# Performance work log

Hardware: AMD Instinct MI355X
Metric: run time of the kernel (lower is better)

Reference implementation:

```python
import jax, jax.numpy as jnp
import numpy as np
from jax import lax

B, T_SRC, I, H, L, O = 1024, 1024, 64, 512, 64, 1


def _lstm_cell(x, h, c, W_ih, W_hh, b):
    # PyTorch gate order: i, f, g, o. b = b_ih + b_hh (same math).
    gates = x @ W_ih.T + h @ W_hh.T + b  # (B, 4H)
    i, f, g, o = jnp.split(gates, 4, axis=-1)
    c_new = jax.nn.sigmoid(f) * c + jax.nn.sigmoid(i) * jnp.tanh(g)
    h_new = jax.nn.sigmoid(o) * jnp.tanh(c_new)
    return h_new, c_new


def setup_inputs() -> dict:
    key = jax.random.key(0)
    ks = jax.random.split(key, 16)
    s_e = 1.0 / np.sqrt(H)
    inp = {
        "src": jax.random.normal(ks[0], (B, T_SRC, I), dtype=jnp.float32),
        "eps": jax.random.normal(ks[1], (B, L), dtype=jnp.float32),
        "tgt_len": 1024,
        # encoder LSTM
        "W_ih_e": jax.random.uniform(ks[2], (4 * H, I), jnp.float32, -s_e, s_e),
        "W_hh_e": jax.random.uniform(ks[3], (4 * H, H), jnp.float32, -s_e, s_e),
        "b_e": jax.random.uniform(ks[4], (4 * H,), jnp.float32, -s_e, s_e),
        # fc_mu / fc_logvar
        "W_mu": jax.random.uniform(ks[5], (L, H), jnp.float32, -s_e, s_e),
        "b_mu": jax.random.uniform(ks[6], (L,), jnp.float32, -s_e, s_e),
        "W_lv": jax.random.uniform(ks[7], (L, H), jnp.float32, -s_e, s_e),
        "b_lv": jax.random.uniform(ks[8], (L,), jnp.float32, -s_e, s_e),
        # z -> h0, c0
        "W_zh": jax.random.uniform(ks[9], (H, L), jnp.float32, -s_e, s_e),
        "b_zh": jax.random.uniform(ks[10], (H,), jnp.float32, -s_e, s_e),
        "W_zc": jax.random.uniform(ks[11], (H, L), jnp.float32, -s_e, s_e),
        "b_zc": jax.random.uniform(ks[12], (H,), jnp.float32, -s_e, s_e),
        # decoder LSTM + fc_out
        "W_ih_d": jax.random.uniform(ks[13], (4 * H, O), jnp.float32, -s_e, s_e),
        "W_hh_d": jax.random.uniform(ks[14], (4 * H, H), jnp.float32, -s_e, s_e),
        "b_d": jax.random.uniform(ks[15], (4 * H,), jnp.float32, -s_e, s_e),
        "W_out": jax.random.uniform(jax.random.fold_in(key, 100), (O, H), jnp.float32, -s_e, s_e),
        "b_out": jax.random.uniform(jax.random.fold_in(key, 101), (O,), jnp.float32, -s_e, s_e),
    }
    return inp


def reference(src, eps, W_ih_e, W_hh_e, b_e, W_mu, b_mu, W_lv, b_lv,
              W_zh, b_zh, W_zc, b_zc, W_ih_d, W_hh_d, b_d, W_out, b_out,
              tgt_len):
    batch = src.shape[0]
    hid = W_hh_e.shape[1]

    # ---- Encoder: LSTM over src, take final hidden state ----
    def enc_step(carry, x_t):
        h, c = carry
        h, c = _lstm_cell(x_t, h, c, W_ih_e, W_hh_e, b_e)
        return (h, c), None

    h0 = jnp.zeros((batch, hid), src.dtype)
    (h_n, _), _ = lax.scan(enc_step, (h0, h0), jnp.swapaxes(src, 0, 1))

    mu = h_n @ W_mu.T + b_mu          # (B, L)
    logvar = h_n @ W_lv.T + b_lv      # (B, L)

    # ---- Reparameterize ----
    z = mu + eps * jnp.exp(0.5 * logvar)

    h_d = jnp.tanh(z @ W_zh.T + b_zh)
    c_d = jnp.tanh(z @ W_zc.T + b_zc)
    x0 = jnp.zeros((batch, W_ih_d.shape[1]), src.dtype)  # (B, output_size)

    def dec_step(carry, _):
        h, c, x = carry
        h, c = _lstm_cell(x, h, c, W_ih_d, W_hh_d, b_d)
        out = h @ W_out.T + b_out     # (B, O)
        return (h, c, out), out

    _, outs = lax.scan(dec_step, (h_d, c_d, x0), None, length=tgt_len)
    recon = jnp.swapaxes(outs, 0, 1)  # (B, tgt_len, O)
    return recon, mu, logvar
```

## Files before the change

### kernel.cpp

```cpp
#include <hip/hip_runtime.h>


#define NWG  256
#define NTHR 256

typedef __attribute__((ext_vector_type(8))) short short8;
typedef __attribute__((ext_vector_type(4))) float f32x4;
typedef __attribute__((ext_vector_type(4))) unsigned int u32x4;

constexpr int Bt = 1024;
constexpr int Tt = 1024;
constexpr int In = 64;
constexpr int Hn = 512;
constexpr int Ln = 64;
constexpr int KE = In + Hn;
constexpr int BSE = KE + 8;
constexpr int KD = Hn;
constexpr int BSD = KD + 8;
constexpr int LDS_BYTES = 128 * BSE * 2;
constexpr int AP_MI = 16 * Hn;

__device__ __forceinline__ float bf2f(unsigned short s){
  unsigned u = ((unsigned)s) << 16; float f; __builtin_memcpy(&f, &u, 4); return f;
}
__device__ __forceinline__ unsigned short f2bf(float f){
  unsigned u; __builtin_memcpy(&u, &f, 4);
  u += 0x7FFFu + ((u >> 16) & 1u);
  return (unsigned short)(u >> 16);
}
__device__ __forceinline__ float sigm(float x){ return 1.0f / (1.0f + __expf(-x)); }
__device__ __forceinline__ float tanh_(float x){ float e = __expf(2.0f * x); return 1.0f - 2.0f / (e + 1.0f); }

__device__ __forceinline__ u32x4 ldcc(const void* p){
  u32x4 r;
  asm volatile("global_load_dwordx4 %0, %1, off sc0 sc1" : "=&v"(r) : "v"(p) : "memory");
  return r;
}
__device__ __forceinline__ float ld32cc(const void* p){
  float r;
  asm volatile("global_load_dword %0, %1, off sc0 sc1" : "=&v"(r) : "v"(p) : "memory");
  return r;
}
__device__ __forceinline__ void st16cc(void* p, unsigned v){
  asm volatile("global_store_short %0, %1, off sc0 sc1" :: "v"(p), "v"(v) : "memory");
}
__device__ __forceinline__ void st32cc(void* p, float v){
  asm volatile("global_store_dword %0, %1, off sc0 sc1" :: "v"(p), "v"(v) : "memory");
}
__device__ __forceinline__ void st128cc(void* p, u32x4 v){
  asm volatile("global_store_dwordx4 %0, %1, off sc0 sc1" :: "v"(p), "v"(v) : "memory");
}

__device__ __forceinline__ void group_sync(unsigned* cnt, unsigned target){
  asm volatile("s_waitcnt vmcnt(0)" ::: "memory");
  __syncthreads();
  if (threadIdx.x == 0){
    __hip_atomic_fetch_add(cnt, 1u, __ATOMIC_RELAXED, __HIP_MEMORY_SCOPE_AGENT);
    while (__hip_atomic_load(cnt, __ATOMIC_RELAXED, __HIP_MEMORY_SCOPE_AGENT) < target)
      __builtin_amdgcn_s_sleep(2);
  }
  __syncthreads();
}

#define SB0 __builtin_amdgcn_sched_barrier(0)

#define LOADC(P, CBASE) do{                                              \
    _Pragma("unroll") for (int ti_ = 0; ti_ < 4; ++ti_){                 \
      A[P][ti_][0] = ldcc(ap + (CBASE) + ti_ * 32);                      \
      A[P][ti_][1] = ldcc(ap + AP_MI + (CBASE) + ti_ * 32);              \
    } }while(0)

#define WAITC(P, N) do{                                                  \
    asm volatile("s_waitcnt vmcnt(" N ")"                                \
      : "+v"(A[P][0][0]), "+v"(A[P][0][1]), "+v"(A[P][1][0]),            \
        "+v"(A[P][1][1]), "+v"(A[P][2][0]), "+v"(A[P][2][1]),            \
        "+v"(A[P][3][0]), "+v"(A[P][3][1]) :: "memory");                 \
    SB0; }while(0)

#define COMPC(P, K0, BB, BS) do{                                         \
    _Pragma("unroll") for (int ti_ = 0; ti_ < 4; ++ti_){                 \
      short8 a0_ = __builtin_bit_cast(short8, A[P][ti_][0]);             \
      short8 a1_ = __builtin_bit_cast(short8, A[P][ti_][1]);             \
      _Pragma("unroll") for (int ni_ = 0; ni_ < 4; ++ni_){               \
        short8 bv_ = *(const short8*)((BB) + ni_ * 16 * (BS) + (K0) + ti_ * 32); \
        acc[0][ni_] = __builtin_amdgcn_mfma_f32_16x16x32_bf16(a0_, bv_, acc[0][ni_], 0, 0, 0); \
        acc[1][ni_] = __builtin_amdgcn_mfma_f32_16x16x32_bf16(a1_, bv_, acc[1][ni_], 0, 0, 0); \
      } } }while(0)

extern "C" __global__ void __launch_bounds__(NTHR, 1)
vae_fused(const float* __restrict__ src, const float* __restrict__ eps,
          const float* __restrict__ Wih_e, const float* __restrict__ Whh_e, const float* __restrict__ b_e,
          const float* __restrict__ Wmu, const float* __restrict__ bmu,
          const float* __restrict__ Wlv, const float* __restrict__ blv,
          const float* __restrict__ Wzh, const float* __restrict__ bzh,
          const float* __restrict__ Wzc, const float* __restrict__ bzc,
          const float* __restrict__ Wih_d, const float* __restrict__ Whh_d, const float* __restrict__ b_d,
          const float* __restrict__ Wout, const float* __restrict__ bout,
          float* __restrict__ out,
          unsigned* cnt_all, unsigned short* hbuf0, unsigned short* hbuf1,
          float* zbuf, float* obuf)
{
  const int tid  = threadIdx.x;
  const int wg   = blockIdx.x;
  const int lane = tid & 63;
  const int wave = tid >> 6;
  const int wm   = wave >> 1, wn = wave & 1;
  const int mt   = wg & 15;
  const int nt   = wg >> 4;
  unsigned* cnt  = cnt_all + mt * 32;
  unsigned bars  = 0;

  extern __shared__ short bpanel[];

  const int l15   = lane & 15;
  const int l4    = lane >> 4;
  const int kq    = l4 * 8;
  const int jcol  = nt * 32 + wn * 16 + l15;
  const int arow0 = mt * 64 + wm * 32 + l15;
  const int brow0 = mt * 64 + wm * 32 + l4 * 4;

  {
    const int idx = nt * NTHR + tid;
    const u32x4 z = {0u, 0u, 0u, 0u};
    st128cc(hbuf0 + (size_t)(mt * 64 + (idx >> 6)) * Hn + (idx & 63) * 8, z);
  }
  for (int idx = tid; idx < 128 * KE; idx += NTHR){
    int q = idx / KE;
    int k = idx - q * KE;
    int gate = (q >> 4) & 3, jl = q & 15, wnn = (q >> 6) & 1;
    int j = nt * 32 + wnn * 16 + jl;
    int r = gate * Hn + j;
    float v = (k < In) ? Wih_e[r * In + k] : Whh_e[(size_t)r * Hn + (k - In)];
    bpanel[q * BSE + k] = (short)f2bf(v);
  }
  float biasr[4], wihr[4];
  #pragma unroll
  for (int ni = 0; ni < 4; ++ni) biasr[ni] = b_e[ni * Hn + jcol];
  bars += 16; group_sync(cnt, bars);

  float c[2][4] = {{0.f,0.f,0.f,0.f},{0.f,0.f,0.f,0.f}};
  const f32x4 fz = {0.f, 0.f, 0.f, 0.f};
  u32x4 A[2][4][2];

  for (int t = 0; t < Tt; ++t){
    const unsigned short* hs = (t & 1) ? hbuf1 : hbuf0;
    unsigned short*       hd = (t & 1) ? hbuf0 : hbuf1;
    f32x4 acc[2][4];
    #pragma unroll
    for (int mi = 0; mi < 2; ++mi)
      #pragma unroll
      for (int ni = 0; ni < 4; ++ni) acc[mi][ni] = fz;

    const short* bbase = bpanel + (wn * 64 + l15) * BSE + kq;

    short8 sa[2][2];
    #pragma unroll
    for (int mi = 0; mi < 2; ++mi){
      const float* sp = src + ((size_t)(arow0 + mi * 16) * Tt + t) * In + kq;
      f32x4 f0 = *(const f32x4*)sp;
      f32x4 f1 = *(const f32x4*)(sp + 4);
      f32x4 f2 = *(const f32x4*)(sp + 32);
      f32x4 f3 = *(const f32x4*)(sp + 36);
      short8 a0, a1;
      #pragma unroll
      for (int e = 0; e < 4; ++e){
        a0[e] = (short)f2bf(f0[e]); a0[4 + e] = (short)f2bf(f1[e]);
        a1[e] = (short)f2bf(f2[e]); a1[4 + e] = (short)f2bf(f3[e]);
      }
      sa[mi][0] = a0; sa[mi][1] = a1;
    }

    const unsigned short* ap = hs + (size_t)arow0 * Hn + kq;
    LOADC(0, 0); LOADC(1, 128);

    #pragma unroll
    for (int kk = 0; kk < 2; ++kk)
      #pragma unroll
      for (int ni = 0; ni < 4; ++ni){
        short8 bv = *(const short8*)(bbase + ni * 16 * BSE + kk * 32);
        acc[0][ni] = __builtin_amdgcn_mfma_f32_16x16x32_bf16(sa[0][kk], bv, acc[0][ni], 0, 0, 0);
        acc[1][ni] = __builtin_amdgcn_mfma_f32_16x16x32_bf16(sa[1][kk], bv, acc[1][ni], 0, 0, 0);
      }

    WAITC(0, "8"); COMPC(0, In + 0,   bbase, BSE);
    LOADC(0, 256);
    WAITC(1, "8"); COMPC(1, In + 128, bbase, BSE);
    LOADC(1, 384);
    WAITC(0, "8"); COMPC(0, In + 256, bbase, BSE);
    WAITC(1, "0"); COMPC(1, In + 384, bbase, BSE);

    #pragma unroll
    for (int mi = 0; mi < 2; ++mi){
      #pragma unroll
      for (int r = 0; r < 4; ++r){
        float gi = acc[mi][0][r] + biasr[0];
        float gf = acc[mi][1][r] + biasr[1];
        float gg = acc[mi][2][r] + biasr[2];
        float go = acc[mi][3][r] + biasr[3];
        float cn = sigm(gf) * c[mi][r] + sigm(gi) * tanh_(gg);
        c[mi][r] = cn;
        float hn = sigm(go) * tanh_(cn);
        st16cc(hd + (size_t)(brow0 + mi * 16 + r) * Hn + jcol, (unsigned)f2bf(hn));
      }
    }
    bars += 16; group_sync(cnt, bars);
  }

  {
    const int lt = nt * NTHR + tid;
    const int b  = mt * 64 + (lt >> 6);
    const int l  = lt & 63;
    const unsigned short* hp = hbuf0 + (size_t)b * Hn;
    const float* wmrow = Wmu + l * Hn;
    const float* wlrow = Wlv + l * Hn;
    float smu = 0.f, slv = 0.f;
    for (int jj = 0; jj < Hn; jj += 32){
      u32x4 v0 = ldcc(hp + jj), v1 = ldcc(hp + jj + 8), v2 = ldcc(hp + jj + 16), v3 = ldcc(hp + jj + 24);
      asm volatile("s_waitcnt vmcnt(0)" : "+v"(v0), "+v"(v1), "+v"(v2), "+v"(v3) :: "memory");
      short8 h0 = __builtin_bit_cast(short8, v0);
      short8 h1 = __builtin_bit_cast(short8, v1);
      short8 h2 = __builtin_bit_cast(short8, v2);
      short8 h3 = __builtin_bit_cast(short8, v3);
      #pragma unroll
      for (int e = 0; e < 8; ++e){
        float f0 = bf2f((unsigned short)h0[e]), f1 = bf2f((unsigned short)h1[e]);
        float f2 = bf2f((unsigned short)h2[e]), f3 = bf2f((unsigned short)h3[e]);
        smu = __builtin_fmaf(f0, wmrow[jj + e], smu);      slv = __builtin_fmaf(f0, wlrow[jj + e], slv);
        smu = __builtin_fmaf(f1, wmrow[jj + 8 + e], smu);  slv = __builtin_fmaf(f1, wlrow[jj + 8 + e], slv);
        smu = __builtin_fmaf(f2, wmrow[jj + 16 + e], smu); slv = __builtin_fmaf(f2, wlrow[jj + 16 + e], slv);
        smu = __builtin_fmaf(f3, wmrow[jj + 24 + e], smu); slv = __builtin_fmaf(f3, wlrow[jj + 24 + e], slv);
      }
    }
    smu += bmu[l]; slv += blv[l];
    out[(size_t)Bt * Tt + (size_t)b * Ln + l] = smu;
    out[(size_t)Bt * Tt + (size_t)Bt * Ln + (size_t)b * Ln + l] = slv;
    st32cc(zbuf + (size_t)b * Ln + l, smu + eps[(size_t)b * Ln + l] * __expf(0.5f * slv));
  }
  bars += 16; group_sync(cnt, bars);

  for (int idx = tid; idx < 128 * KD; idx += NTHR){
    int q = idx >> 9, k = idx & 511;
    int gate = (q >> 4) & 3, jl = q & 15, wnn = (q >> 6) & 1;
    int j = nt * 32 + wnn * 16 + jl;
    bpanel[q * BSD + k] = (short)f2bf(Whh_d[(size_t)(gate * Hn + j) * Hn + k]);
  }
  #pragma unroll
  for (int ni = 0; ni < 4; ++ni){
    biasr[ni] = b_d[ni * Hn + jcol];
    wihr[ni]  = Wih_d[ni * Hn + jcol];
  }
  const float woutr = Wout[jcol];
  const float bov   = bout[0];
  #pragma unroll
  for (int mi = 0; mi < 2; ++mi){
    #pragma unroll
    for (int r = 0; r < 4; ++r){
      int b = brow0 + mi * 16 + r;
      const float* zp  = zbuf + (size_t)b * Ln;
      const float* whr = Wzh + jcol * Ln;
      const float* wcr = Wzc + jcol * Ln;
      float sh = bzh[jcol], sc = bzc[jcol];
      for (int e0 = 0; e0 < Ln; e0 += 16){
        u32x4 z0 = ldcc(zp + e0), z1 = ldcc(zp + e0 + 4), z2 = ldcc(zp + e0 + 8), z3 = ldcc(zp + e0 + 12);
        asm volatile("s_waitcnt vmcnt(0)" : "+v"(z0), "+v"(z1), "+v"(z2), "+v"(z3) :: "memory");
        f32x4 zf0 = __builtin_bit_cast(f32x4, z0);
        f32x4 zf1 = __builtin_bit_cast(f32x4, z1);
        f32x4 zf2 = __builtin_bit_cast(f32x4, z2);
        f32x4 zf3 = __builtin_bit_cast(f32x4, z3);
        #pragma unroll
        for (int e = 0; e < 4; ++e){
          sh = __builtin_fmaf(zf0[e], whr[e0 + e], sh);      sc = __builtin_fmaf(zf0[e], wcr[e0 + e], sc);
          sh = __builtin_fmaf(zf1[e], whr[e0 + 4 + e], sh);  sc = __builtin_fmaf(zf1[e], wcr[e0 + 4 + e], sc);
          sh = __builtin_fmaf(zf2[e], whr[e0 + 8 + e], sh);  sc = __builtin_fmaf(zf2[e], wcr[e0 + 8 + e], sc);
          sh = __builtin_fmaf(zf3[e], whr[e0 + 12 + e], sh); sc = __builtin_fmaf(zf3[e], wcr[e0 + 12 + e], sc);
        }
      }
      c[mi][r] = tanh_(sc);
      st16cc(hbuf0 + (size_t)b * Hn + jcol, (unsigned)f2bf(tanh_(sh)));
    }
  }
  if (nt == 0 && tid < 3 * 64)
    st32cc(obuf + (tid >> 6) * Bt + mt * 64 + (tid & 63), bov);
  bars += 16; group_sync(cnt, bars);

  for (int t = 0; t < Tt; ++t){
    const unsigned short* hs = (t & 1) ? hbuf1 : hbuf0;
    unsigned short*       hd = (t & 1) ? hbuf0 : hbuf1;
    float*       oacc  = obuf + (t % 3) * Bt;
    const float* oread = obuf + ((t + 2) % 3) * Bt;
    float*       orst  = obuf + ((t + 1) % 3) * Bt;

    if (nt == 0){
      if (t > 0 && tid < 64){
        float v = ld32cc(oread + mt * 64 + tid);
        asm volatile("s_waitcnt vmcnt(0)" : "+v"(v) :: "memory");
        out[(size_t)(mt * 64 + tid) * Tt + (t - 1)] = v;
      }
      if (tid < 64) st32cc(orst + mt * 64 + tid, bov);
    }

    float xv[2][4];
    #pragma unroll
    for (int mi = 0; mi < 2; ++mi)
      #pragma unroll
      for (int r = 0; r < 4; ++r)
        xv[mi][r] = ld32cc(oread + brow0 + mi * 16 + r);

    f32x4 acc[2][4];
    #pragma unroll
    for (int mi = 0; mi < 2; ++mi)
      #pragma unroll
      for (int ni = 0; ni < 4; ++ni) acc[mi][ni] = fz;

    const short* bbase = bpanel + (wn * 64 + l15) * BSD + kq;
    const unsigned short* ap = hs + (size_t)arow0 * Hn + kq;

    LOADC(0, 0); LOADC(1, 128);
    WAITC(0, "8"); COMPC(0, 0,   bbase, BSD);
    LOADC(0, 256);
    WAITC(1, "8"); COMPC(1, 128, bbase, BSD);
    LOADC(1, 384);
    WAITC(0, "8"); COMPC(0, 256, bbase, BSD);
    WAITC(1, "0"); COMPC(1, 384, bbase, BSD);

    asm volatile("s_waitcnt vmcnt(0)"
      : "+v"(xv[0][0]), "+v"(xv[0][1]), "+v"(xv[0][2]), "+v"(xv[0][3]),
        "+v"(xv[1][0]), "+v"(xv[1][1]), "+v"(xv[1][2]), "+v"(xv[1][3]) :: "memory");

    #pragma unroll
    for (int mi = 0; mi < 2; ++mi){
      #pragma unroll
      for (int r = 0; r < 4; ++r){
        float x = (t == 0) ? 0.f : xv[mi][r];
        float gi = acc[mi][0][r] + biasr[0] + x * wihr[0];
        float gf = acc[mi][1][r] + biasr[1] + x * wihr[1];
        float gg = acc[mi][2][r] + biasr[2] + x * wihr[2];
        float go = acc[mi][3][r] + biasr[3] + x * wihr[3];
        float cn = sigm(gf) * c[mi][r] + sigm(gi) * tanh_(gg);
        c[mi][r] = cn;
        float hn = sigm(go) * tanh_(cn);
        int b = brow0 + mi * 16 + r;
        st16cc(hd + (size_t)b * Hn + jcol, (unsigned)f2bf(hn));
        float pv = hn * woutr;
        pv += __shfl_xor(pv, 1);
        pv += __shfl_xor(pv, 2);
        pv += __shfl_xor(pv, 4);
        pv += __shfl_xor(pv, 8);
        if (l15 == 0)
          __hip_atomic_fetch_add(&oacc[b], pv, __ATOMIC_RELAXED, __HIP_MEMORY_SCOPE_AGENT);
      }
    }
    bars += 16; group_sync(cnt, bars);
  }
  if (nt == 0 && tid < 64){
    float v = ld32cc(obuf + 0 * Bt + mt * 64 + tid);
    asm volatile("s_waitcnt vmcnt(0)" : "+v"(v) :: "memory");
    out[(size_t)(mt * 64 + tid) * Tt + (Tt - 1)] = v;
  }
}

extern "C" void kernel_launch(void* const* d_in, const int* in_sizes, int n_in,
                              void* d_out, int out_size, void* d_ws, size_t ws_size,
                              hipStream_t stream){
  (void)in_sizes; (void)n_in; (void)out_size; (void)ws_size;
  const float* src   = (const float*)d_in[0];
  const float* eps   = (const float*)d_in[1];
  const float* Wih_e = (const float*)d_in[3];
  const float* Whh_e = (const float*)d_in[4];
  const float* b_e   = (const float*)d_in[5];
  const float* Wmu   = (const float*)d_in[6];
  const float* bmu   = (const float*)d_in[7];
  const float* Wlv   = (const float*)d_in[8];
  const float* blv   = (const float*)d_in[9];
  const float* Wzh   = (const float*)d_in[10];
  const float* bzh   = (const float*)d_in[11];
  const float* Wzc   = (const float*)d_in[12];
  const float* bzc   = (const float*)d_in[13];
  const float* Wih_d = (const float*)d_in[14];
  const float* Whh_d = (const float*)d_in[15];
  const float* b_d   = (const float*)d_in[16];
  const float* Wout  = (const float*)d_in[17];
  const float* bout  = (const float*)d_in[18];

  char* ws = (char*)d_ws;
  unsigned*       cnt  = (unsigned*)ws;
  unsigned short* h0   = (unsigned short*)(ws + 4096);
  unsigned short* h1   = (unsigned short*)(ws + 4096 + 1048576);
  float*          zbuf = (float*)(ws + 4096 + 2 * 1048576);
  float*          obuf = (float*)(ws + 4096 + 2 * 1048576 + 262144);

  hipFuncSetAttribute((const void*)vae_fused,
                      hipFuncAttributeMaxDynamicSharedMemorySize, LDS_BYTES);
  hipMemsetAsync(cnt, 0, 2048, stream);
  hipLaunchKernelGGL(vae_fused, dim3(NWG), dim3(NTHR), LDS_BYTES, stream,
                     src, eps, Wih_e, Whh_e, b_e, Wmu, bmu, Wlv, blv,
                     Wzh, bzh, Wzc, bzc, Wih_d, Whh_d, b_d, Wout, bout,
                     (float*)d_out, cnt, h0, h1, zbuf, obuf);
}
```

Baseline: 16.65 ms.

## Detect same-XCD groups to relax cache coherence bits; issue all h loads upfront

At startup each workgroup records its XCC id and checks whether all 16 workgroups sharing an M-tile sit on the same XCD. If they do, the hidden-state loads and stores drop the sc1 system-coherence bit and keep only sc0, so they can be served from the shared L2 instead of bypassing it. The kernel body is templated on this flag. The h-state loads are also issued as four chunks up front, rather than in two double-buffered pairs, and use immediate offsets; src loads become inline asm so they overlap with the h loads. This uses more registers, and if workgroups from one group land on different XCDs the kernel falls back to the fully coherent path.

```diff
diff --git a/kernel.cpp b/kernel.cpp
--- a/kernel.cpp
+++ b/kernel.cpp
@@ -8,11 +8,7 @@
 typedef __attribute__((ext_vector_type(4))) float f32x4;
 typedef __attribute__((ext_vector_type(4))) unsigned int u32x4;
 
-constexpr int Bt = 1024;
-constexpr int Tt = 1024;
-constexpr int In = 64;
-constexpr int Hn = 512;
-constexpr int Ln = 64;
+constexpr int Bt = 1024, Tt = 1024, In = 64, Hn = 512, Ln = 64;
 constexpr int KE = In + Hn;
 constexpr int BSE = KE + 8;
 constexpr int KD = Hn;
@@ -20,6 +16,8 @@
 constexpr int LDS_BYTES = 128 * BSE * 2;
 constexpr int AP_MI = 16 * Hn;
 
+template<bool B> struct BoolC { static constexpr bool value = B; };
+
 __device__ __forceinline__ float bf2f(unsigned short s){
   unsigned u = ((unsigned)s) << 16; float f; __builtin_memcpy(&f, &u, 4); return f;
 }
@@ -31,24 +29,58 @@
 __device__ __forceinline__ float sigm(float x){ return 1.0f / (1.0f + __expf(-x)); }
 __device__ __forceinline__ float tanh_(float x){ float e = __expf(2.0f * x); return 1.0f - 2.0f / (e + 1.0f); }
 
-__device__ __forceinline__ u32x4 ldcc(const void* p){
+template<bool SAME, int OFF>
+__device__ __forceinline__ u32x4 ldA(const void* p){
   u32x4 r;
-  asm volatile("global_load_dwordx4 %0, %1, off sc0 sc1" : "=&v"(r) : "v"(p) : "memory");
+  if constexpr (SAME) asm volatile("global_load_dwordx4 %0, %1, off offset:%c2 sc0" : "=&v"(r) : "v"(p), "i"(OFF));
+  else                asm volatile("global_load_dwordx4 %0, %1, off offset:%c2 sc0 sc1" : "=&v"(r) : "v"(p), "i"(OFF));
   return r;
 }
-__device__ __forceinline__ float ld32cc(const void* p){
+template<int OFF>
+__device__ __forceinline__ u32x4 ldP(const void* p){
+  u32x4 r;
+  asm volatile("global_load_dwordx4 %0, %1, off offset:%c2" : "=&v"(r) : "v"(p), "i"(OFF));
+  return r;
+}
+template<bool SAME>
+__device__ __forceinline__ float ld32w(const void* p){
   float r;
+  if constexpr (SAME) asm volatile("global_load_dword %0, %1, off sc0" : "=&v"(r) : "v"(p));
+  else                asm volatile("global_load_dword %0, %1, off sc0 sc1" : "=&v"(r) : "v"(p));
+  asm volatile("s_waitcnt vmcnt(0)" : "+v"(r));
+  return r;
+}
+template<bool SAME>
+__device__ __forceinline__ void st16(void* p, unsigned v){
+  if constexpr (SAME) asm volatile("global_store_short %0, %1, off sc0" :: "v"(p), "v"(v) : "memory");
+  else                asm volatile("global_store_short %0, %1, off sc0 sc1" :: "v"(p), "v"(v) : "memory");
+}
+template<bool SAME>
+__device__ __forceinline__ void st32(void* p, float v){
+  if constexpr (SAME) asm volatile("global_store_dword %0, %1, off sc0" :: "v"(p), "v"(v) : "memory");
+  else                asm volatile("global_store_dword %0, %1, off sc0 sc1" :: "v"(p), "v"(v) : "memory");
+}
+template<bool SAME>
+__device__ __forceinline__ void st128(void* p, u32x4 v){
+  if constexpr (SAME) asm volatile("global_store_dwordx4 %0, %1, off sc0" :: "v"(p), "v"(v) : "memory");
+  else                asm volatile("global_store_dwordx4 %0, %1, off sc0 sc1" :: "v"(p), "v"(v) : "memory");
+}
+__device__ __forceinline__ void stP32(void* p, float v){
+  asm volatile("global_store_dword %0, %1, off" :: "v"(p), "v"(v) : "memory");
+}
+template<bool SAME>
+__device__ __forceinline__ void atomAddF(float* p, float v){
+  if constexpr (SAME) asm volatile("global_atomic_add_f32 %0, %1, off" :: "v"(p), "v"(v) : "memory");
+  else                asm volatile("global_atomic_add_f32 %0, %1, off sc1" :: "v"(p), "v"(v) : "memory");
+}
+__device__ __forceinline__ unsigned ldMall(const unsigned* p){
+  unsigned r;
   asm volatile("global_load_dword %0, %1, off sc0 sc1" : "=&v"(r) : "v"(p) : "memory");
+  asm volatile("s_waitcnt vmcnt(0)" : "+v"(r) :: "memory");
   return r;
 }
-__device__ __forceinline__ void st16cc(void* p, unsigned v){
-  asm volatile("global_store_short %0, %1, off sc0 sc1" :: "v"(p), "v"(v) : "memory");
-}
-__device__ __forceinline__ void st32cc(void* p, float v){
+__device__ __forceinline__ void stMall(unsigned* p, unsigned v){
   asm volatile("global_store_dword %0, %1, off sc0 sc1" :: "v"(p), "v"(v) : "memory");
-}
-__device__ __forceinline__ void st128cc(void* p, u32x4 v){
-  asm volatile("global_store_dwordx4 %0, %1, off sc0 sc1" :: "v"(p), "v"(v) : "memory");
 }
 
 __device__ __forceinline__ void group_sync(unsigned* cnt, unsigned target){
@@ -62,27 +94,25 @@
   __syncthreads();
 }
 
-#define SB0 __builtin_amdgcn_sched_barrier(0)
-
-#define LOADC(P, CBASE) do{                                              \
-    _Pragma("unroll") for (int ti_ = 0; ti_ < 4; ++ti_){                 \
-      A[P][ti_][0] = ldcc(ap + (CBASE) + ti_ * 32);                      \
-      A[P][ti_][1] = ldcc(ap + AP_MI + (CBASE) + ti_ * 32);              \
-    } }while(0)
-
-#define WAITC(P, N) do{                                                  \
-    asm volatile("s_waitcnt vmcnt(" N ")"                                \
-      : "+v"(A[P][0][0]), "+v"(A[P][0][1]), "+v"(A[P][1][0]),            \
-        "+v"(A[P][1][1]), "+v"(A[P][2][0]), "+v"(A[P][2][1]),            \
-        "+v"(A[P][3][0]), "+v"(A[P][3][1]) :: "memory");                 \
-    SB0; }while(0)
-
-#define COMPC(P, K0, BB, BS) do{                                         \
-    _Pragma("unroll") for (int ti_ = 0; ti_ < 4; ++ti_){                 \
-      short8 a0_ = __builtin_bit_cast(short8, A[P][ti_][0]);             \
-      short8 a1_ = __builtin_bit_cast(short8, A[P][ti_][1]);             \
-      _Pragma("unroll") for (int ni_ = 0; ni_ < 4; ++ni_){               \
-        short8 bv_ = *(const short8*)((BB) + ni_ * 16 * (BS) + (K0) + ti_ * 32); \
+template<bool SAME, int CB>
+__device__ __forceinline__ void loadChunk(const unsigned short* a0, const unsigned short* a1,
+                                          u32x4 (&d)[4][2]){
+  d[0][0] = ldA<SAME, (CB +  0) * 2>(a0);  d[0][1] = ldA<SAME, (CB +  0) * 2>(a1);
+  d[1][0] = ldA<SAME, (CB + 32) * 2>(a0);  d[1][1] = ldA<SAME, (CB + 32) * 2>(a1);
+  d[2][0] = ldA<SAME, (CB + 64) * 2>(a0);  d[2][1] = ldA<SAME, (CB + 64) * 2>(a1);
+  d[3][0] = ldA<SAME, (CB + 96) * 2>(a0);  d[3][1] = ldA<SAME, (CB + 96) * 2>(a1);
+}
+
+#define TIEC(C) "+v"(A[C][0][0]), "+v"(A[C][0][1]), "+v"(A[C][1][0]), "+v"(A[C][1][1]), \
+                "+v"(A[C][2][0]), "+v"(A[C][2][1]), "+v"(A[C][3][0]), "+v"(A[C][3][1])
+#define WAITC(C, N) asm volatile("s_waitcnt vmcnt(" N ")" : TIEC(C))
+
+#define COMPC(C, K0, BS) do{                                                     \
+    _Pragma("unroll") for (int ti_ = 0; ti_ < 4; ++ti_){                         \
+      short8 a0_ = __builtin_bit_cast(short8, A[C][ti_][0]);                     \
+      short8 a1_ = __builtin_bit_cast(short8, A[C][ti_][1]);                     \
+      _Pragma("unroll") for (int ni_ = 0; ni_ < 4; ++ni_){                       \
+        short8 bv_ = *(const short8*)(bbase + ni_ * 16 * (BS) + (K0) + ti_ * 32);\
         acc[0][ni_] = __builtin_amdgcn_mfma_f32_16x16x32_bf16(a0_, bv_, acc[0][ni_], 0, 0, 0); \
         acc[1][ni_] = __builtin_amdgcn_mfma_f32_16x16x32_bf16(a1_, bv_, acc[1][ni_], 0, 0, 0); \
       } } }while(0)
@@ -97,7 +127,8 @@
           const float* __restrict__ Wih_d, const float* __restrict__ Whh_d, const float* __restrict__ b_d,
           const float* __restrict__ Wout, const float* __restrict__ bout,
           float* __restrict__ out,
-          unsigned* cnt_all, unsigned short* hbuf0, unsigned short* hbuf1,
+          unsigned* cnt_all, unsigned* xcdbuf,
+          unsigned short* hbuf0, unsigned short* hbuf1,
           float* zbuf, float* obuf)
 {
   const int tid  = threadIdx.x;
@@ -111,6 +142,7 @@
   unsigned bars  = 0;
 
   extern __shared__ short bpanel[];
+  __shared__ unsigned s_same;
 
   const int l15   = lane & 15;
   const int l4    = lane >> 4;
@@ -119,244 +151,271 @@
   const int arow0 = mt * 64 + wm * 32 + l15;
   const int brow0 = mt * 64 + wm * 32 + l4 * 4;
 
-  {
-    const int idx = nt * NTHR + tid;
-    const u32x4 z = {0u, 0u, 0u, 0u};
-    st128cc(hbuf0 + (size_t)(mt * 64 + (idx >> 6)) * Hn + (idx & 63) * 8, z);
+  unsigned xcc;
+  asm volatile("s_getreg_b32 %0, hwreg(HW_REG_XCC_ID)" : "=s"(xcc));
+  if (tid == 0) stMall(xcdbuf + mt * 16 + nt, xcc + 1u);
+  bars += 16; group_sync(cnt, bars);
+  if (tid < 64){
+    unsigned v = xcc + 1u;
+    if (tid < 16) v = ldMall(xcdbuf + mt * 16 + tid);
+    unsigned long long bl = __ballot(v == xcc + 1u);
+    if (tid == 0) s_same = (bl == ~0ull) ? 1u : 0u;
   }
-  for (int idx = tid; idx < 128 * KE; idx += NTHR){
-    int q = idx / KE;
-    int k = idx - q * KE;
-    int gate = (q >> 4) & 3, jl = q & 15, wnn = (q >> 6) & 1;
-    int j = nt * 32 + wnn * 16 + jl;
-    int r = gate * Hn + j;
-    float v = (k < In) ? Wih_e[r * In + k] : Whh_e[(size_t)r * Hn + (k - In)];
-    bpanel[q * BSE + k] = (short)f2bf(v);
-  }
-  float biasr[4], wihr[4];
-  #pragma unroll
-  for (int ni = 0; ni < 4; ++ni) biasr[ni] = b_e[ni * Hn + jcol];
-  bars += 16; group_sync(cnt, bars);
-
-  float c[2][4] = {{0.f,0.f,0.f,0.f},{0.f,0.f,0.f,0.f}};
-  const f32x4 fz = {0.f, 0.f, 0.f, 0.f};
-  u32x4 A[2][4][2];
-
-  for (int t = 0; t < Tt; ++t){
-    const unsigned short* hs = (t & 1) ? hbuf1 : hbuf0;
-    unsigned short*       hd = (t & 1) ? hbuf0 : hbuf1;
-    f32x4 acc[2][4];
+  __syncthreads();
+  const bool same_xcd = (s_same != 0u);
+
+  auto body = [&](auto SC){
+    constexpr bool SAME = decltype(SC)::value;
+
+    {
+      const int idx = nt * NTHR + tid;
+      const u32x4 z = {0u, 0u, 0u, 0u};
+      st128<SAME>(hbuf0 + (size_t)(mt * 64 + (idx >> 6)) * Hn + (idx & 63) * 8, z);
+    }
+    for (int idx = tid; idx < 128 * KE; idx += NTHR){
+      int q = idx / KE;
+      int k = idx - q * KE;
+      int gate = (q >> 4) & 3, jl = q & 15, wnn = (q >> 6) & 1;
+      int j = nt * 32 + wnn * 16 + jl;
+      int r = gate * Hn + j;
+      float v = (k < In) ? Wih_e[r * In + k] : Whh_e[(size_t)r * Hn + (k - In)];
+      bpanel[q * BSE + k] = (short)f2bf(v);
+    }
+    float biasr[4], wihr[4];
     #pragma unroll
-    for (int mi = 0; mi < 2; ++mi)
-      #pragma unroll
-      for (int ni = 0; ni < 4; ++ni) acc[mi][ni] = fz;
-
-    const short* bbase = bpanel + (wn * 64 + l15) * BSE + kq;
-
-    short8 sa[2][2];
+    for (int ni = 0; ni < 4; ++ni) biasr[ni] = b_e[ni * Hn + jcol];
+    bars += 16; group_sync(cnt, bars);
+
+    float c[2][4] = {{0.f,0.f,0.f,0.f},{0.f,0.f,0.f,0.f}};
+    const f32x4 fz = {0.f, 0.f, 0.f, 0.f};
+    u32x4 A[4][4][2];
+
+    for (int t = 0; t < Tt; ++t){
+      const unsigned short* hs = (t & 1) ? hbuf1 : hbuf0;
+      unsigned short*       hd = (t & 1) ? hbuf0 : hbuf1;
+
+      const float* sp0 = src + ((size_t)arow0 * Tt + t) * In + kq;
+      const float* sp1 = src + ((size_t)(arow0 + 16) * Tt + t) * In + kq;
+      u32x4 sv[2][4];
+      sv[0][0] = ldP<0>(sp0); sv[0][1] = ldP<16>(sp0); sv[0][2] = ldP<128>(sp0); sv[0][3] = ldP<144>(sp0);
+      sv[1][0] = ldP<0>(sp1); sv[1][1] = ldP<16>(sp1); sv[1][2] = ldP<128>(sp1); sv[1][3] = ldP<144>(sp1);
+
+      const unsigned short* ap0 = hs + (size_t)arow0 * Hn + kq;
+      const unsigned short* ap1 = ap0 + AP_MI;
+      loadChunk<SAME,   0>(ap0, ap1, A[0]);
+      loadChunk<SAME, 128>(ap0, ap1, A[1]);
+      loadChunk<SAME, 256>(ap0, ap1, A[2]);
+      loadChunk<SAME, 384>(ap0, ap1, A[3]);
+
+      asm volatile("s_waitcnt vmcnt(32)"
+        : "+v"(sv[0][0]), "+v"(sv[0][1]), "+v"(sv[0][2]), "+v"(sv[0][3]),
+          "+v"(sv[1][0]), "+v"(sv[1][1]), "+v"(sv[1][2]), "+v"(sv[1][3]));
+      short8 sa[2][2];
+      #pragma unroll
+      for (int mi = 0; mi < 2; ++mi){
+        f32x4 f0 = __builtin_bit_cast(f32x4, sv[mi][0]);
+        f32x4 f1 = __builtin_bit_cast(f32x4, sv[mi][1]);
+        f32x4 f2 = __builtin_bit_cast(f32x4, sv[mi][2]);
+        f32x4 f3 = __builtin_bit_cast(f32x4, sv[mi][3]);
+        short8 a0, a1;
+        #pragma unroll
+        for (int e = 0; e < 4; ++e){
+          a0[e] = (short)f2bf(f0[e]); a0[4 + e] = (short)f2bf(f1[e]);
+          a1[e] = (short)f2bf(f2[e]); a1[4 + e] = (short)f2bf(f3[e]);
+        }
+        sa[mi][0] = a0; sa[mi][1] = a1;
+      }
+
+      f32x4 acc[2][4];
+      #pragma unroll
+      for (int mi = 0; mi < 2; ++mi)
+        #pragma unroll
+        for (int ni = 0; ni < 4; ++ni) acc[mi][ni] = fz;
+
+      const short* bbase = bpanel + (wn * 64 + l15) * BSE + kq;
+      #pragma unroll
+      for (int kk = 0; kk < 2; ++kk)
+        #pragma unroll
+        for (int ni = 0; ni < 4; ++ni){
+          short8 bv = *(const short8*)(bbase + ni * 16 * BSE + kk * 32);
+          acc[0][ni] = __builtin_amdgcn_mfma_f32_16x16x32_bf16(sa[0][kk], bv, acc[0][ni], 0, 0, 0);
+          acc[1][ni] = __builtin_amdgcn_mfma_f32_16x16x32_bf16(sa[1][kk], bv, acc[1][ni], 0, 0, 0);
+        }
+
+      WAITC(0, "24"); COMPC(0, In +   0, BSE);
+      WAITC(1, "16"); COMPC(1, In + 128, BSE);
+      WAITC(2,  "8"); COMPC(2, In + 256, BSE);
+      WAITC(3,  "0"); COMPC(3, In + 384, BSE);
+
+      #pragma unroll
+      for (int mi = 0; mi < 2; ++mi){
+        #pragma unroll
+        for (int r = 0; r < 4; ++r){
+          float gi = acc[mi][0][r] + biasr[0];
+          float gf = acc[mi][1][r] + biasr[1];
+          float gg = acc[mi][2][r] + biasr[2];
+          float go = acc[mi][3][r] + biasr[3];
+          float cn = sigm(gf) * c[mi][r] + sigm(gi) * tanh_(gg);
+          c[mi][r] = cn;
+          float hn = sigm(go) * tanh_(cn);
+          st16<SAME>(hd + (size_t)(brow0 + mi * 16 + r) * Hn + jcol, (unsigned)f2bf(hn));
+        }
+      }
+      bars += 16; group_sync(cnt, bars);
+    }
+
+    {
+      const int lt = nt * NTHR + tid;
+      const int b  = mt * 64 + (lt >> 6);
+      const int l  = lt & 63;
+      const unsigned short* hp = hbuf0 + (size_t)b * Hn;
+      const float* wmrow = Wmu + l * Hn;
+      const float* wlrow = Wlv + l * Hn;
+      float smu = 0.f, slv = 0.f;
+      for (int jj = 0; jj < Hn; jj += 32){
+        u32x4 v0 = ldA<SAME,0>(hp + jj),      v1 = ldA<SAME,16>(hp + jj);
+        u32x4 v2 = ldA<SAME,32>(hp + jj),     v3 = ldA<SAME,48>(hp + jj);
+        asm volatile("s_waitcnt vmcnt(0)" : "+v"(v0), "+v"(v1), "+v"(v2), "+v"(v3));
+        short8 h0 = __builtin_bit_cast(short8, v0);
+        short8 h1 = __builtin_bit_cast(short8, v1);
+        short8 h2 = __builtin_bit_cast(short8, v2);
+        short8 h3 = __builtin_bit_cast(short8, v3);
+        #pragma unroll
+        for (int e = 0; e < 8; ++e){
+          float f0 = bf2f((unsigned short)h0[e]), f1 = bf2f((unsigned short)h1[e]);
+          float f2 = bf2f((unsigned short)h2[e]), f3 = bf2f((unsigned short)h3[e]);
+          smu = __builtin_fmaf(f0, wmrow[jj + e], smu);      slv = __builtin_fmaf(f0, wlrow[jj + e], slv);
+          smu = __builtin_fmaf(f1, wmrow[jj + 8 + e], smu);  slv = __builtin_fmaf(f1, wlrow[jj + 8 + e], slv);
+          smu = __builtin_fmaf(f2, wmrow[jj + 16 + e], smu); slv = __builtin_fmaf(f2, wlrow[jj + 16 + e], slv);
+          smu = __builtin_fmaf(f3, wmrow[jj + 24 + e], smu); slv = __builtin_fmaf(f3, wlrow[jj + 24 + e], slv);
+        }
+      }
+      smu += bmu[l]; slv += blv[l];
+      out[(size_t)Bt * Tt + (size_t)b * Ln + l] = smu;
+      out[(size_t)Bt * Tt + (size_t)Bt * Ln + (size_t)b * Ln + l] = slv;
+      st32<SAME>(zbuf + (size_t)b * Ln + l, smu + eps[(size_t)b * Ln + l] * __expf(0.5f * slv));
+    }
+    bars += 16; group_sync(cnt, bars);
+
+    for (int idx = tid; idx < 128 * KD; idx += NTHR){
+      int q = idx >> 9, k = idx & 511;
+      int gate = (q >> 4) & 3, jl = q & 15, wnn = (q >> 6) & 1;
+      int j = nt * 32 + wnn * 16 + jl;
+      bpanel[q * BSD + k] = (short)f2bf(Whh_d[(size_t)(gate * Hn + j) * Hn + k]);
+    }
+    #pragma unroll
+    for (int ni = 0; ni < 4; ++ni){
+      biasr[ni] = b_d[ni * Hn + jcol];
+      wihr[ni]  = Wih_d[ni * Hn + jcol];
+    }
+    const float woutr = Wout[jcol];
+    const float bov   = bout[0];
     #pragma unroll
     for (int mi = 0; mi < 2; ++mi){
-      const float* sp = src + ((size_t)(arow0 + mi * 16) * Tt + t) * In + kq;
-      f32x4 f0 = *(const f32x4*)sp;
-      f32x4 f1 = *(const f32x4*)(sp + 4);
-      f32x4 f2 = *(const f32x4*)(sp + 32);
-      f32x4 f3 = *(const f32x4*)(sp + 36);
-      short8 a0, a1;
-      #pragma unroll
-      for (int e = 0; e < 4; ++e){
-        a0[e] = (short)f2bf(f0[e]); a0[4 + e] = (short)f2bf(f1[e]);
-        a1[e] = (short)f2bf(f2[e]); a1[4 + e] = (short)f2bf(f3[e]);
-      }
-      sa[mi][0] = a0; sa[mi][1] = a1;
-    }
-
-    const unsigned short* ap = hs + (size_t)arow0 * Hn + kq;
-    LOADC(0, 0); LOADC(1, 128);
-
-    #pragma unroll
-    for (int kk = 0; kk < 2; ++kk)
-      #pragma unroll
-      for (int ni = 0; ni < 4; ++ni){
-        short8 bv = *(const short8*)(bbase + ni * 16 * BSE + kk * 32);
-        acc[0][ni] = __builtin_amdgcn_mfma_f32_16x16x32_bf16(sa[0][kk], bv, acc[0][ni], 0, 0, 0);
-        acc[1][ni] = __builtin_amdgcn_mfma_f32_16x16x32_bf16(sa[1][kk], bv, acc[1][ni], 0, 0, 0);
-      }
-
-    WAITC(0, "8"); COMPC(0, In + 0,   bbase, BSE);
-    LOADC(0, 256);
-    WAITC(1, "8"); COMPC(1, In + 128, bbase, BSE);
-    LOADC(1, 384);
-    WAITC(0, "8"); COMPC(0, In + 256, bbase, BSE);
-    WAITC(1, "0"); COMPC(1, In + 384, bbase, BSE);
-
-    #pragma unroll
-    for (int mi = 0; mi < 2; ++mi){
       #pragma unroll
       for (int r = 0; r < 4; ++r){
-        float gi = acc[mi][0][r] + biasr[0];
-        float gf = acc[mi][1][r] + biasr[1];
-        float gg = acc[mi][2][r] + biasr[2];
-        float go = acc[mi][3][r] + biasr[3];
-        float cn = sigm(gf) * c[mi][r] + sigm(gi) * tanh_(gg);
-        c[mi][r] = cn;
-        float hn = sigm(go) * tanh_(cn);
-        st16cc(hd + (size_t)(brow0 + mi * 16 + r) * Hn + jcol, (unsigned)f2bf(hn));
-      }
-    }
+        int b = brow0 + mi * 16 + r;
+        const float* zp  = zbuf + (size_t)b * Ln;
+        const float* whr = Wzh + jcol * Ln;
+        const float* wcr = Wzc + jcol * Ln;
+        float sh = bzh[jcol], sc = bzc[jcol];
+        for (int e0 = 0; e0 < Ln; e0 += 16){
+          u32x4 z0 = ldA<SAME,0>(zp + e0),  z1 = ldA<SAME,16>(zp + e0);
+          u32x4 z2 = ldA<SAME,32>(zp + e0), z3 = ldA<SAME,48>(zp + e0);
+          asm volatile("s_waitcnt vmcnt(0)" : "+v"(z0), "+v"(z1), "+v"(z2), "+v"(z3));
+          f32x4 zf0 = __builtin_bit_cast(f32x4, z0);
+          f32x4 zf1 = __builtin_bit_cast(f32x4, z1);
+          f32x4 zf2 = __builtin_bit_cast(f32x4, z2);
+          f32x4 zf3 = __builtin_bit_cast(f32x4, z3);
+          #pragma unroll
+          for (int e = 0; e < 4; ++e){
+            sh = __builtin_fmaf(zf0[e], whr[e0 + e], sh);      sc = __builtin_fmaf(zf0[e], wcr[e0 + e], sc);
+            sh = __builtin_fmaf(zf1[e], whr[e0 + 4 + e], sh);  sc = __builtin_fmaf(zf1[e], wcr[e0 + 4 + e], sc);
+            sh = __builtin_fmaf(zf2[e], whr[e0 + 8 + e], sh);  sc = __builtin_fmaf(zf2[e], wcr[e0 + 8 + e], sc);
+            sh = __builtin_fmaf(zf3[e], whr[e0 + 12 + e], sh); sc = __builtin_fmaf(zf3[e], wcr[e0 + 12 + e], sc);
+          }
+        }
+        c[mi][r] = tanh_(sc);
+        st16<SAME>(hbuf0 + (size_t)b * Hn + jcol, (unsigned)f2bf(tanh_(sh)));
+      }
+    }
+    if (nt == 0 && tid < 3 * 64)
+      st32<SAME>(obuf + (tid >> 6) * Bt + mt * 64 + (tid & 63), bov);
     bars += 16; group_sync(cnt, bars);
-  }
-
-  {
-    const int lt = nt * NTHR + tid;
-    const int b  = mt * 64 + (lt >> 6);
-    const int l  = lt & 63;
-    const unsigned short* hp = hbuf0 + (size_t)b * Hn;
-    const float* wmrow = Wmu + l * Hn;
-    const float* wlrow = Wlv + l * Hn;
-    float smu = 0.f, slv = 0.f;
-    for (int jj = 0; jj < Hn; jj += 32){
-      u32x4 v0 = ldcc(hp + jj), v1 = ldcc(hp + jj + 8), v2 = ldcc(hp + jj + 16), v3 = ldcc(hp + jj + 24);
-      asm volatile("s_waitcnt vmcnt(0)" : "+v"(v0), "+v"(v1), "+v"(v2), "+v"(v3) :: "memory");
-      short8 h0 = __builtin_bit_cast(short8, v0);
-      short8 h1 = __builtin_bit_cast(short8, v1);
-      short8 h2 = __builtin_bit_cast(short8, v2);
-      short8 h3 = __builtin_bit_cast(short8, v3);
-      #pragma unroll
-      for (int e = 0; e < 8; ++e){
-        float f0 = bf2f((unsigned short)h0[e]), f1 = bf2f((unsigned short)h1[e]);
-        float f2 = bf2f((unsigned short)h2[e]), f3 = bf2f((unsigned short)h3[e]);
-        smu = __builtin_fmaf(f0, wmrow[jj + e], smu);      slv = __builtin_fmaf(f0, wlrow[jj + e], slv);
-        smu = __builtin_fmaf(f1, wmrow[jj + 8 + e], smu);  slv = __builtin_fmaf(f1, wlrow[jj + 8 + e], slv);
-        smu = __builtin_fmaf(f2, wmrow[jj + 16 + e], smu); slv = __builtin_fmaf(f2, wlrow[jj + 16 + e], slv);
-        smu = __builtin_fmaf(f3, wmrow[jj + 24 + e], smu); slv = __builtin_fmaf(f3, wlrow[jj + 24 + e], slv);
-      }
-    }
-    smu += bmu[l]; slv += blv[l];
-    out[(size_t)Bt * Tt + (size_t)b * Ln + l] = smu;
-    out[(size_t)Bt * Tt + (size_t)Bt * Ln + (size_t)b * Ln + l] = slv;
-    st32cc(zbuf + (size_t)b * Ln + l, smu + eps[(size_t)b * Ln + l] * __expf(0.5f * slv));
-  }
-  bars += 16; group_sync(cnt, bars);
-
-  for (int idx = tid; idx < 128 * KD; idx += NTHR){
-    int q = idx >> 9, k = idx & 511;
-    int gate = (q >> 4) & 3, jl = q & 15, wnn = (q >> 6) & 1;
-    int j = nt * 32 + wnn * 16 + jl;
-    bpanel[q * BSD + k] = (short)f2bf(Whh_d[(size_t)(gate * Hn + j) * Hn + k]);
-  }
-  #pragma unroll
-  for (int ni = 0; ni < 4; ++ni){
-    biasr[ni] = b_d[ni * Hn + jcol];
-    wihr[ni]  = Wih_d[ni * Hn + jcol];
-  }
-  const float woutr = Wout[jcol];
-  const float bov   = bout[0];
-  #pragma unroll
-  for (int mi = 0; mi < 2; ++mi){
-    #pragma unroll
-    for (int r = 0; r < 4; ++r){
-      int b = brow0 + mi * 16 + r;
-      const float* zp  = zbuf + (size_t)b * Ln;
-      const float* whr = Wzh + jcol * Ln;
-      const float* wcr = Wzc + jcol * Ln;
-      float sh = bzh[jcol], sc = bzc[jcol];
-      for (int e0 = 0; e0 < Ln; e0 += 16){
-        u32x4 z0 = ldcc(zp + e0), z1 = ldcc(zp + e0 + 4), z2 = ldcc(zp + e0 + 8), z3 = ldcc(zp + e0 + 12);
-        asm volatile("s_waitcnt vmcnt(0)" : "+v"(z0), "+v"(z1), "+v"(z2), "+v"(z3) :: "memory");
-        f32x4 zf0 = __builtin_bit_cast(f32x4, z0);
-        f32x4 zf1 = __builtin_bit_cast(f32x4, z1);
-        f32x4 zf2 = __builtin_bit_cast(f32x4, z2);
-        f32x4 zf3 = __builtin_bit_cast(f32x4, z3);
-        #pragma unroll
-        for (int e = 0; e < 4; ++e){
-          sh = __builtin_fmaf(zf0[e], whr[e0 + e], sh);      sc = __builtin_fmaf(zf0[e], wcr[e0 + e], sc);
-          sh = __builtin_fmaf(zf1[e], whr[e0 + 4 + e], sh);  sc = __builtin_fmaf(zf1[e], wcr[e0 + 4 + e], sc);
-          sh = __builtin_fmaf(zf2[e], whr[e0 + 8 + e], sh);  sc = __builtin_fmaf(zf2[e], wcr[e0 + 8 + e], sc);
-          sh = __builtin_fmaf(zf3[e], whr[e0 + 12 + e], sh); sc = __builtin_fmaf(zf3[e], wcr[e0 + 12 + e], sc);
-        }
-      }
-      c[mi][r] = tanh_(sc);
-      st16cc(hbuf0 + (size_t)b * Hn + jcol, (unsigned)f2bf(tanh_(sh)));
-    }
-  }
-  if (nt == 0 && tid < 3 * 64)
-    st32cc(obuf + (tid >> 6) * Bt + mt * 64 + (tid & 63), bov);
-  bars += 16; group_sync(cnt, bars);
-
-  for (int t = 0; t < Tt; ++t){
-    const unsigned short* hs = (t & 1) ? hbuf1 : hbuf0;
-    unsigned short*       hd = (t & 1) ? hbuf0 : hbuf1;
-    float*       oacc  = obuf + (t % 3) * Bt;
-    const float* oread = obuf + ((t + 2) % 3) * Bt;
-    float*       orst  = obuf + ((t + 1) % 3) * Bt;
-
-    if (nt == 0){
-      if (t > 0 && tid < 64){
-        float v = ld32cc(oread + mt * 64 + tid);
-        asm volatile("s_waitcnt vmcnt(0)" : "+v"(v) :: "memory");
-        out[(size_t)(mt * 64 + tid) * Tt + (t - 1)] = v;
-      }
-      if (tid < 64) st32cc(orst + mt * 64 + tid, bov);
-    }
-
-    float xv[2][4];
-    #pragma unroll
-    for (int mi = 0; mi < 2; ++mi)
-      #pragma unroll
-      for (int r = 0; r < 4; ++r)
-        xv[mi][r] = ld32cc(oread + brow0 + mi * 16 + r);
-
-    f32x4 acc[2][4];
-    #pragma unroll
-    for (int mi = 0; mi < 2; ++mi)
-      #pragma unroll
-      for (int ni = 0; ni < 4; ++ni) acc[mi][ni] = fz;
-
-    const short* bbase = bpanel + (wn * 64 + l15) * BSD + kq;
-    const unsigned short* ap = hs + (size_t)arow0 * Hn + kq;
-
-    LOADC(0, 0); LOADC(1, 128);
-    WAITC(0, "8"); COMPC(0, 0,   bbase, BSD);
-    LOADC(0, 256);
-    WAITC(1, "8"); COMPC(1, 128, bbase, BSD);
-    LOADC(1, 384);
-    WAITC(0, "8"); COMPC(0, 256, bbase, BSD);
-    WAITC(1, "0"); COMPC(1, 384, bbase, BSD);
-
-    asm volatile("s_waitcnt vmcnt(0)"
-      : "+v"(xv[0][0]), "+v"(xv[0][1]), "+v"(xv[0][2]), "+v"(xv[0][3]),
-        "+v"(xv[1][0]), "+v"(xv[1][1]), "+v"(xv[1][2]), "+v"(xv[1][3]) :: "memory");
-
-    #pragma unroll
-    for (int mi = 0; mi < 2; ++mi){
-      #pragma unroll
-      for (int r = 0; r < 4; ++r){
-        float x = (t == 0) ? 0.f : xv[mi][r];
-        float gi = acc[mi][0][r] + biasr[0] + x * wihr[0];
-        float gf = acc[mi][1][r] + biasr[1] + x * wihr[1];
-        float gg = acc[mi][2][r] + biasr[2] + x * wihr[2];
-        float go = acc[mi][3][r] + biasr[3] + x * wihr[3];
-        float cn = sigm(gf) * c[mi][r] + sigm(gi) * tanh_(gg);
-        c[mi][r] = cn;
-        float hn = sigm(go) * tanh_(cn);
-        int b = brow0 + mi * 16 + r;
-        st16cc(hd + (size_t)b * Hn + jcol, (unsigned)f2bf(hn));
-        float pv = hn * woutr;
-        pv += __shfl_xor(pv, 1);
-        pv += __shfl_xor(pv, 2);
-        pv += __shfl_xor(pv, 4);
-        pv += __shfl_xor(pv, 8);
-        if (l15 == 0)
-          __hip_atomic_fetch_add(&oacc[b], pv, __ATOMIC_RELAXED, __HIP_MEMORY_SCOPE_AGENT);
-      }
-    }
-    bars += 16; group_sync(cnt, bars);
-  }
-  if (nt == 0 && tid < 64){
-    float v = ld32cc(obuf + 0 * Bt + mt * 64 + tid);
-    asm volatile("s_waitcnt vmcnt(0)" : "+v"(v) :: "memory");
-    out[(size_t)(mt * 64 + tid) * Tt + (Tt - 1)] = v;
-  }
+
+    for (int t = 0; t < Tt; ++t){
+      const unsigned short* hs = (t & 1) ? hbuf1 : hbuf0;
+      unsigned short*       hd = (t & 1) ? hbuf0 : hbuf1;
+      float*       oacc  = obuf + (t % 3) * Bt;
+      const float* oread = obuf + ((t + 2) % 3) * Bt;
+      float*       orst  = obuf + ((t + 1) % 3) * Bt;
+
+      if (nt == 0){
+        if (t > 0 && tid < 64){
+          float v = ld32w<SAME>(oread + mt * 64 + tid);
+          stP32(out + (size_t)(mt * 64 + tid) * Tt + (t - 1), v);
+        }
+        if (tid < 64) st32<SAME>(orst + mt * 64 + tid, bov);
+      }
+
+      u32x4 xvv[2];
+      xvv[0] = ldA<SAME, 0>(oread + brow0);
+      xvv[1] = ldA<SAME, 64>(oread + brow0);
+
+      const unsigned short* ap0 = hs + (size_t)arow0 * Hn + kq;
+      const unsigned short* ap1 = ap0 + AP_MI;
+      loadChunk<SAME,   0>(ap0, ap1, A[0]);
+      loadChunk<SAME, 128>(ap0, ap1, A[1]);
+      loadChunk<SAME, 256>(ap0, ap1, A[2]);
+      loadChunk<SAME, 384>(ap0, ap1, A[3]);
+
+      f32x4 acc[2][4];
+      #pragma unroll
+      for (int mi = 0; mi < 2; ++mi)
+        #pragma unroll
+        for (int ni = 0; ni < 4; ++ni) acc[mi][ni] = fz;
+
+      const short* bbase = bpanel + (wn * 64 + l15) * BSD + kq;
+      WAITC(0, "24"); COMPC(0,   0, BSD);
+      WAITC(1, "16"); COMPC(1, 128, BSD);
+      WAITC(2,  "8"); COMPC(2, 256, BSD);
+      WAITC(3,  "0"); COMPC(3, 384, BSD);
+      asm volatile("s_waitcnt vmcnt(0)" : "+v"(xvv[0]), "+v"(xvv[1]));
+      f32x4 xf0 = __builtin_bit_cast(f32x4, xvv[0]);
+      f32x4 xf1 = __builtin_bit_cast(f32x4, xvv[1]);
+
+      #pragma unroll
+      for (int mi = 0; mi < 2; ++mi){
+        #pragma unroll
+        for (int r = 0; r < 4; ++r){
+          float x = (t == 0) ? 0.f : (mi == 0 ? xf0[r] : xf1[r]);
+          float gi = acc[mi][0][r] + biasr[0] + x * wihr[0];
+          float gf = acc[mi][1][r] + biasr[1] + x * wihr[1];
+          float gg = acc[mi][2][r] + biasr[2] + x * wihr[2];
+          float go = acc[mi][3][r] + biasr[3] + x * wihr[3];
+          float cn = sigm(gf) * c[mi][r] + sigm(gi) * tanh_(gg);
+          c[mi][r] = cn;
+          float hn = sigm(go) * tanh_(cn);
+          int b = brow0 + mi * 16 + r;
+          st16<SAME>(hd + (size_t)b * Hn + jcol, (unsigned)f2bf(hn));
+          float pv = hn * woutr;
+          pv += __shfl_xor(pv, 1);
+          pv += __shfl_xor(pv, 2);
+          pv += __shfl_xor(pv, 4);
+          pv += __shfl_xor(pv, 8);
+          if (l15 == 0) atomAddF<SAME>(&oacc[b], pv);
+        }
+      }
+      bars += 16; group_sync(cnt, bars);
+    }
+    if (nt == 0 && tid < 64){
+      float v = ld32w<SAME>(obuf + 0 * Bt + mt * 64 + tid);
+      stP32(out + (size_t)(mt * 64 + tid) * Tt + (Tt - 1), v);
+    }
+  };
+
+  if (same_xcd) body(BoolC<true>{});
+  else          body(BoolC<false>{});
 }
 
 extern "C" void kernel_launch(void* const* d_in, const int* in_sizes, int n_in,
@@ -383,17 +442,18 @@
   const float* bout  = (const float*)d_in[18];
 
   char* ws = (char*)d_ws;
-  unsigned*       cnt  = (unsigned*)ws;
-  unsigned short* h0   = (unsigned short*)(ws + 4096);
-  unsigned short* h1   = (unsigned short*)(ws + 4096 + 1048576);
-  float*          zbuf = (float*)(ws + 4096 + 2 * 1048576);
-  float*          obuf = (float*)(ws + 4096 + 2 * 1048576 + 262144);
+  unsigned*       cnt   = (unsigned*)ws;
+  unsigned*       xcdb  = (unsigned*)(ws + 2048);
+  unsigned short* h0    = (unsigned short*)(ws + 4096);
+  unsigned short* h1    = (unsigned short*)(ws + 4096 + 1048576);
+  float*          zbuf  = (float*)(ws + 4096 + 2 * 1048576);
+  float*          obuf  = (float*)(ws + 4096 + 2 * 1048576 + 262144);
 
   hipFuncSetAttribute((const void*)vae_fused,
                       hipFuncAttributeMaxDynamicSharedMemorySize, LDS_BYTES);
-  hipMemsetAsync(cnt, 0, 2048, stream);
+  (void)hipMemsetAsync(ws, 0, 4096, stream);
   hipLaunchKernelGGL(vae_fused, dim3(NWG), dim3(NTHR), LDS_BYTES, stream,
                      src, eps, Wih_e, Whh_e, b_e, Wmu, bmu, Wlv, blv,
                      Wzh, bzh, Wzc, bzc, Wih_d, Whh_d, b_d, Wout, bout,
-                     (float*)d_out, cnt, h0, h1, zbuf, obuf);
-}
+                     (float*)d_out, cnt, xcdb, h0, h1, zbuf, obuf);
+}
```

Result: slower. 23.97 ms (+43.9%).
